# Kernel tuning notes

Measured on AMD Instinct MI355X. Metric: run time of the kernel, lower is better.

Reference implementation:

```python
import jax, jax.numpy as jnp
import numpy as np

B, N, S = 8, 4096, 1024
D1, D2 = 128, 256
IN_C = D1 + D2
MLP = [256, 256]
BN_EPS = 1e-5


def setup_inputs() -> dict:
    key = jax.random.key(0)
    ks = jax.random.split(key, 32)
    inp = {
        'xyz1': jax.random.uniform(ks[0], (B, 3, N), dtype=jnp.float32),
        'xyz2': jax.random.uniform(ks[1], (B, 3, S), dtype=jnp.float32),
        'points1': jax.random.normal(ks[2], (B, D1, N), dtype=jnp.float32),
        'points2': jax.random.normal(ks[3], (B, D2, S), dtype=jnp.float32),
        'colors1': jax.random.normal(ks[4], (B, D1, N), dtype=jnp.float32),
        'colors2': jax.random.normal(ks[5], (B, D2, S), dtype=jnp.float32),
    }
    # conv1x1 + BN params for the two MLP stacks (points / colors)
    k = 6
    last = IN_C
    for li, out_c in enumerate(MLP, start=1):
        for tag in ('p', 'c'):
            scale = 1.0 / np.sqrt(last)
            inp[f'W{tag}{li}'] = jax.random.uniform(ks[k], (out_c, last), jnp.float32, -scale, scale); k += 1
            inp[f'b{tag}{li}'] = jax.random.uniform(ks[k], (out_c,), jnp.float32, -scale, scale); k += 1
            inp[f'g{tag}{li}'] = jnp.ones((out_c,), jnp.float32)
            inp[f'be{tag}{li}'] = jnp.zeros((out_c,), jnp.float32)
        last = out_c
    return inp


def _square_distance(src, dst):
    # src [B,N,3], dst [B,S,3] -> [B,N,S]
    d = -2.0 * jnp.einsum('bnc,bsc->bns', src, dst)
    d = d + jnp.sum(src * src, -1)[:, :, None]
    d = d + jnp.sum(dst * dst, -1)[:, None, :]
    return d


def _three_interp(xyz1, xyz2, feat2):
    # xyz1 [B,N,3], xyz2 [B,S,3], feat2 [B,S,D] -> [B,N,D]
    dists = _square_distance(xyz1, xyz2)              # [B,N,S]
    neg_d3, idx = jax.lax.top_k(-dists, 3)            # smallest 3 distances
    d3 = -neg_d3                                      # [B,N,3] ascending
    recip = 1.0 / (d3 + 1e-8)
    weight = recip / jnp.sum(recip, axis=2, keepdims=True)
    gathered = jax.vmap(lambda f, i: f[i])(feat2, idx)  # [B,N,3,D]
    return jnp.sum(gathered * weight[..., None], axis=2)


def _conv_bn_relu(x, W, b, g, be):
    # x [B,N,Cin]; conv1x1 == per-point linear; BN in training mode (batch stats)
    y = jnp.einsum('bnc,oc->bno', x, W) + b
    m = jnp.mean(y, axis=(0, 1))
    v = jnp.var(y, axis=(0, 1))
    yn = (y - m) * jax.lax.rsqrt(v + BN_EPS)
    return jax.nn.relu(yn * g + be)


def reference(xyz1, xyz2, points1, points2, colors1, colors2,
              Wp1, bp1, gp1, bep1, Wc1, bc1, gc1, bec1,
              Wp2, bp2, gp2, bep2, Wc2, bc2, gc2, bec2):
    x1 = jnp.transpose(xyz1, (0, 2, 1))   # [B,N,3]
    x2 = jnp.transpose(xyz2, (0, 2, 1))   # [B,S,3]
    p2 = jnp.transpose(points2, (0, 2, 1))  # [B,S,D2]
    c2 = jnp.transpose(colors2, (0, 2, 1))

    interp_p = _three_interp(x1, x2, p2)  # [B,N,D2]
    interp_c = _three_interp(x1, x2, c2)

    p1 = jnp.transpose(points1, (0, 2, 1))  # [B,N,D1]
    c1 = jnp.transpose(colors1, (0, 2, 1))
    new_p = jnp.concatenate([p1, interp_p], axis=-1)  # [B,N,IN_C]
    new_c = jnp.concatenate([c1, interp_c], axis=-1)

    new_p = _conv_bn_relu(new_p, Wp1, bp1, gp1, bep1)
    new_p = _conv_bn_relu(new_p, Wp2, bp2, gp2, bep2)
    new_c = _conv_bn_relu(new_c, Wc1, bc1, gc1, bec1)
    new_c = _conv_bn_relu(new_c, Wc2, bc2, gc2, bec2)

    return (jnp.transpose(new_p, (0, 2, 1)), jnp.transpose(new_c, (0, 2, 1)))
```

## Files before the change

### kernel.cpp

```cpp
#include <hip/hip_runtime.h>
#include <cstdint>
#include <cstddef>


#define B_   8
#define N_   4096
#define S_   1024
#define D1_  128
#define D2_  256
#define INC_ 384
#define OC_  256
#define M_   (B_ * N_)

typedef __attribute__((ext_vector_type(8))) short sh8;
typedef __attribute__((ext_vector_type(4))) float f32x4;
typedef __attribute__((ext_vector_type(4))) unsigned short ush4;
typedef __attribute__((ext_vector_type(8))) unsigned short ush8;

__device__ __forceinline__ unsigned short bf16rne(float f) {
    union { float f; unsigned u; } v; v.f = f;
    return (unsigned short)((v.u + 0x7FFFu + ((v.u >> 16) & 1u)) >> 16);
}
__device__ __forceinline__ float bf2f(unsigned short h) {
    union { unsigned u; float f; } v; v.u = ((unsigned)h) << 16;
    return v.f;
}
__device__ __forceinline__ void gload16(const void* gsrc, void* lds) {
    __builtin_amdgcn_global_load_lds(
        (const __attribute__((address_space(1))) void*)gsrc,
        (__attribute__((address_space(3))) void*)lds, 16, 0, 0);
}

#define INS(pd, pi) { \
    bool l0 = (pd < d0) || (pd == d0 && pi < i0); \
    bool l1 = (pd < d1) || (pd == d1 && pi < i1); \
    bool l2 = (pd < d2) || (pd == d2 && pi < i2); \
    d2 = l1 ? d1 : (l2 ? pd : d2);  i2 = l1 ? i1 : (l2 ? pi : i2); \
    d1 = l0 ? d0 : (l1 ? pd : d1);  i1 = l0 ? i0 : (l1 ? pi : i1); \
    d0 = l0 ? pd : d0;              i0 = l0 ? pi : i0; \
}

__global__ __launch_bounds__(256) void front_kernel(
    const float* __restrict__ xyz1, const float* __restrict__ xyz2,
    const float* __restrict__ points1, const float* __restrict__ colors1,
    const float* __restrict__ points2, const float* __restrict__ colors2,
    const float* __restrict__ Wp1, const float* __restrict__ Wc1,
    const float* __restrict__ Wp2, const float* __restrict__ Wc2,
    int* __restrict__ idxo, float* __restrict__ wo,
    unsigned short* __restrict__ p2b, unsigned short* __restrict__ c2b,
    unsigned short* __restrict__ Wb1, unsigned short* __restrict__ Wb2,
    unsigned short* __restrict__ Xp)
{
    __shared__ __align__(16) char fsm[17664];
    const int bid = blockIdx.x;
    const int tid = threadIdx.x;

    if (bid < 1024) {
        float4* sc = (float4*)fsm;
        const int b = bid >> 7, qb = bid & 127;
        const float* x2 = xyz2 + (size_t)b * 3 * S_;
        for (int s = tid; s < S_; s += 256) {
            float xs = x2[s], ys = x2[S_ + s], zs = x2[2 * S_ + s];
            sc[s] = make_float4(xs, ys, zs, xs * xs + ys * ys + zs * zs);
        }
        __syncthreads();
        const int q = qb * 32 + (tid >> 3);
        const int sub = tid & 7;
        const float* x1 = xyz1 + (size_t)b * 3 * N_;
        const float xq = x1[q], yq = x1[N_ + q], zq = x1[2 * N_ + q];
        const float n1 = xq * xq + yq * yq + zq * zq;
        float d0 = 3.4e38f, d1 = 3.4e38f, d2 = 3.4e38f;
        int i0 = 0, i1 = 0, i2 = 0;
#pragma unroll 4
        for (int j = 0; j < 128; ++j) {
            int s = j * 8 + sub;
            float4 v = sc[s];
            float dot = xq * v.x + yq * v.y + zq * v.z;
            float d = (n1 - 2.0f * dot) + v.w;
            bool c0 = d < d0, c1 = d < d1, c2 = d < d2;
            d2 = c1 ? d1 : (c2 ? d : d2); i2 = c1 ? i1 : (c2 ? s : i2);
            d1 = c0 ? d0 : (c1 ? d : d1); i1 = c0 ? i0 : (c1 ? s : i1);
            d0 = c0 ? d : d0;             i0 = c0 ? s : i0;
        }
#pragma unroll
        for (int off = 1; off < 8; off <<= 1) {
            float pd0 = __shfl_xor(d0, off), pd1 = __shfl_xor(d1, off), pd2 = __shfl_xor(d2, off);
            int   pi0 = __shfl_xor(i0, off), pi1 = __shfl_xor(i1, off), pi2 = __shfl_xor(i2, off);
            INS(pd0, pi0) INS(pd1, pi1) INS(pd2, pi2)
        }
        if (sub == 0) {
            float r0 = 1.f / (d0 + 1e-8f);
            float r1 = 1.f / (d1 + 1e-8f);
            float r2 = 1.f / (d2 + 1e-8f);
            float rs = r0 + r1 + r2;
            int base = (b * N_ + q) * 3;
            idxo[base] = i0; idxo[base + 1] = i1; idxo[base + 2] = i2;
            wo[base] = r0 / rs; wo[base + 1] = r1 / rs; wo[base + 2] = r2 / rs;
        }
    } else if (bid < 5120) {
        float (*tile)[33] = (float(*)[33])fsm;
        const int u = bid - 1024;
        const int which = u >> 11;
        const int v = u & 2047;
        const int z = v >> 8, rem = v & 255;
        const int cx = rem & 31, ry = rem >> 5;
        const int tx = tid & 31, ty = tid >> 5;
        const float* s = (which ? colors2 : points2) + (size_t)z * D2_ * S_;
        unsigned short* d = (which ? c2b : p2b) + (size_t)z * S_ * D2_;
#pragma unroll
        for (int i = 0; i < 4; ++i)
            tile[ty + i * 8][tx] = s[(size_t)(ry * 32 + ty + i * 8) * S_ + cx * 32 + tx];
        __syncthreads();
#pragma unroll
        for (int i = 0; i < 4; ++i)
            d[(size_t)(cx * 32 + ty + i * 8) * D2_ + ry * 32 + tx] =
                bf16rne(tile[tx][ty + i * 8]);
    } else if (bid < 5440) {
        int e = ((bid - 5120) * 256 + tid) * 4;
        const float* src; unsigned short* dst; int off;
        if (e < 98304)       { src = Wp1; dst = Wb1;          off = e; }
        else if (e < 196608) { src = Wc1; dst = Wb1 + 98304;  off = e - 98304; }
        else if (e < 262144) { src = Wp2; dst = Wb2;          off = e - 196608; }
        else                 { src = Wc2; dst = Wb2 + 65536;  off = e - 262144; }
        float4 v = *(const float4*)(src + off);
        ush4 o; o[0] = bf16rne(v.x); o[1] = bf16rne(v.y); o[2] = bf16rne(v.z); o[3] = bf16rne(v.w);
        *(ush4*)(dst + off) = o;
    } else {
        float (*tileA)[69] = (float(*)[69])fsm;
        const int u = bid - 5440;
        const int t = u >> 9, rem = u & 511;
        const int b = rem >> 6, n0 = (rem & 63) * 64;
        const float* x1 = t ? colors1 : points1;
        size_t mbase = (size_t)t * M_ + (size_t)b * N_ + n0;
#pragma unroll
        for (int ph = 0; ph < 2; ++ph) {
            if (ph) __syncthreads();
#pragma unroll
            for (int it = 0; it < 4; ++it) {
                int fl4 = it * 256 + tid;
                int dl = fl4 >> 4, nl = (fl4 & 15) * 4;
                float4 v = *(const float4*)(x1 + ((size_t)b * D1_ + ph * 64 + dl) * N_ + n0 + nl);
                tileA[nl][dl] = v.x; tileA[nl + 1][dl] = v.y;
                tileA[nl + 2][dl] = v.z; tileA[nl + 3][dl] = v.w;
            }
            __syncthreads();
#pragma unroll
            for (int it = 0; it < 2; ++it) {
                int e8 = it * 256 + tid;
                int r = e8 >> 3, dc = (e8 & 7) * 8;
                ush8 o;
#pragma unroll
                for (int j = 0; j < 8; ++j) o[j] = bf16rne(tileA[r][dc + j]);
                *(ush8*)(Xp + (mbase + r) * D1_ + ph * 64 + dc) = o;
            }
        }
    }
}

__global__ __launch_bounds__(512, 1) void gemm1f_kernel(
    const unsigned short* __restrict__ Xp,
    const unsigned short* __restrict__ p2b,
    const unsigned short* __restrict__ c2b,
    const int* __restrict__ idxw, const float* __restrict__ wgtw,
    const unsigned short* __restrict__ Wb1,
    unsigned short* __restrict__ Y1,
    float* __restrict__ psum, float* __restrict__ psq)
{
    const int wg  = blockIdx.x;
    const int xcd = wg & 7;
    const int t   = xcd & 1;
    const int mt  = (xcd >> 1) * 32 + (wg >> 3);
    const int m0  = mt * 256;
    const int bb  = m0 >> 12;
    const unsigned short* Aw  = Wb1 + (size_t)t * (OC_ * INC_);
    const unsigned short* Xb  = Xp + (size_t)t * M_ * D1_;
    const unsigned short* f2b = t ? c2b : p2b;

    __shared__ __align__(16) char smem[131072];

    const int tid  = threadIdx.x;
    const int lane = tid & 63;
    const int wid  = tid >> 6;
    const int wc   = wid & 3;
    const int wm   = wid >> 2;
    const int srow = tid >> 3;
    const int k8   = (tid & 7) * 8;
    const int sk   = ((tid & 7) ^ (srow & 7)) * 8;
    const int kgrp = (lane >> 4) * 16;

    int gi[4][3]; float gw[4][3];
#pragma unroll
    for (int p = 0; p < 4; ++p) {
        int base = (m0 + p * 64 + srow) * 3;
#pragma unroll
        for (int j = 0; j < 3; ++j) { gi[p][j] = idxw[base + j]; gw[p][j] = wgtw[base + j]; }
    }

    f32x4 acc[4][8];
#pragma unroll
    for (int i = 0; i < 4; ++i)
#pragma unroll
        for (int j = 0; j < 8; ++j) acc[i][j] = f32x4{0.f, 0.f, 0.f, 0.f};

    auto stageA = [&](int buf, int kc) {
#pragma unroll
        for (int p = 0; p < 4; ++p)
            gload16(Aw + (size_t)(p * 64 + srow) * INC_ + kc + sk,
                    smem + buf * 32768 + p * 8192 + wid * 1024);
    };
    auto stageBX = [&](int buf, int kc) {
#pragma unroll
        for (int p = 0; p < 4; ++p)
            gload16(Xb + (size_t)(m0 + p * 64 + srow) * D1_ + kc + sk,
                    smem + 65536 + buf * 32768 + p * 8192 + wid * 1024);
    };
    auto stageBG = [&](int buf, int kc) {
        const int d0k = kc - D1_ + k8;
#pragma unroll
        for (int p = 0; p < 4; ++p) {
            int row = p * 64 + srow;
            ush8 a0 = *(const ush8*)(f2b + ((size_t)bb * S_ + gi[p][0]) * D2_ + d0k);
            ush8 a1 = *(const ush8*)(f2b + ((size_t)bb * S_ + gi[p][1]) * D2_ + d0k);
            ush8 a2 = *(const ush8*)(f2b + ((size_t)bb * S_ + gi[p][2]) * D2_ + d0k);
            ush8 ov;
#pragma unroll
            for (int j = 0; j < 8; ++j)
                ov[j] = bf16rne(gw[p][0] * bf2f(a0[j]) + gw[p][1] * bf2f(a1[j])
                              + gw[p][2] * bf2f(a2[j]));
            *(ush8*)(smem + 65536 + buf * 32768 + row * 128
                     + ((k8 * 2) ^ ((row & 7) << 4))) = ov;
        }
    };
    auto compute = [&](int buf) {
#pragma unroll
        for (int kk = 0; kk < 2; ++kk) {
            sh8 a[4], b[8];
#pragma unroll
            for (int f = 0; f < 4; ++f) {
                int ra = wc * 64 + (lane & 15) + f * 16;
                a[f] = *(const sh8*)(smem + buf * 32768 + ra * 128
                        + ((kk * 64 + kgrp) ^ ((ra & 7) << 4)));
            }
#pragma unroll
            for (int f = 0; f < 8; ++f) {
                int rb = wm * 128 + (lane & 15) + f * 16;
                b[f] = *(const sh8*)(smem + 65536 + buf * 32768 + rb * 128
                        + ((kk * 64 + kgrp) ^ ((rb & 7) << 4)));
            }
#pragma unroll
            for (int fc = 0; fc < 4; ++fc)
#pragma unroll
                for (int fm = 0; fm < 8; ++fm)
                    acc[fc][fm] = __builtin_amdgcn_mfma_f32_16x16x32_bf16(
                        a[fc], b[fm], acc[fc][fm], 0, 0, 0);
        }
    };

    stageA(0, 0); stageBX(0, 0);
    __syncthreads();
    int cur = 0;
    for (int step = 0; step < 6; ++step) {
        int kcn = (step + 1) * 64;
        if (step < 5) {
            stageA(cur ^ 1, kcn);
            if (kcn < D1_) stageBX(cur ^ 1, kcn);
            else           stageBG(cur ^ 1, kcn);
        }
        compute(cur);
        __syncthreads();
        cur ^= 1;
    }

    const int mrow = m0 + wm * 128 + (lane & 15);
    const int chq  = (lane >> 4) * 4;
#pragma unroll
    for (int fm = 0; fm < 8; ++fm)
#pragma unroll
        for (int fc = 0; fc < 4; ++fc) {
            ush4 v;
#pragma unroll
            for (int r = 0; r < 4; ++r) v[r] = bf16rne(acc[fc][fm][r]);
            *(ush4*)(Y1 + ((size_t)t * M_ + mrow + fm * 16) * OC_
                      + wc * 64 + fc * 16 + chq) = v;
        }

    float* sArr = (float*)smem;
    const int contrib = wm * 16 + (lane & 15);
#pragma unroll
    for (int ph = 0; ph < 2; ++ph) {
#pragma unroll
        for (int fc = 0; fc < 4; ++fc) {
            f32x4 s4;
#pragma unroll
            for (int r = 0; r < 4; ++r) {
                float s = 0.f;
#pragma unroll
                for (int fm = 0; fm < 8; ++fm) { float v = acc[fc][fm][r]; s += ph ? v * v : v; }
                s4[r] = s;
            }
            *(f32x4*)&sArr[contrib * 264 + wc * 64 + fc * 16 + chq] = s4;
        }
        __syncthreads();
        if (tid < 256) {
            float s = 0.f;
#pragma unroll
            for (int k = 0; k < 32; ++k) s += sArr[((k + tid) & 31) * 264 + tid];
            (ph ? psq : psum)[((size_t)t * 128 + mt) * 256 + tid] = s;
        }
        __syncthreads();
    }
}

__global__ __launch_bounds__(256) void reduce_kernel(
    const float* __restrict__ psum, const float* __restrict__ psq,
    const float* __restrict__ gp, const float* __restrict__ bep,
    const float* __restrict__ gc, const float* __restrict__ bec,
    float* __restrict__ ss, int layerOff)
{
    const int t = blockIdx.x, cs = blockIdx.y;
    const int tid = threadIdx.x;
    const int cl = tid & 63, grp = tid >> 6;
    const int c = cs * 64 + cl;
    float s = 0.f, q = 0.f;
    for (int k = grp; k < 128; k += 4) {
        s += psum[((size_t)t * 128 + k) * 256 + c];
        q += psq [((size_t)t * 128 + k) * 256 + c];
    }
    __shared__ float ls[4][64], lq[4][64];
    ls[grp][cl] = s; lq[grp][cl] = q;
    __syncthreads();
    if (tid < 64) {
        s = ls[0][cl] + ls[1][cl] + ls[2][cl] + ls[3][cl];
        q = lq[0][cl] + lq[1][cl] + lq[2][cl] + lq[3][cl];
        float mean = s * (1.f / (float)M_);
        float var  = q * (1.f / (float)M_) - mean * mean;
        float inv  = rsqrtf(var + 1e-5f);
        float g = (t ? gc : gp)[c], be = (t ? bec : bep)[c];
        float sc = g * inv;
        ss[layerOff + t * 256 + c]       = sc;
        ss[layerOff + 512 + t * 256 + c] = be - mean * sc;
    }
}

__global__ __launch_bounds__(512, 1) void gemm2f_kernel(
    const unsigned short* __restrict__ Y1,
    const unsigned short* __restrict__ Wb2,
    const float* __restrict__ ss,
    unsigned short* __restrict__ y2b,
    float* __restrict__ psum, float* __restrict__ psq)
{
    const int t  = blockIdx.y;
    const int m0 = blockIdx.x * 256;
    const unsigned short* Aw = Wb2 + (size_t)t * (OC_ * OC_);
    const unsigned short* By = Y1 + (size_t)t * M_ * OC_;

    __shared__ __align__(16) char smem[131072];
    __shared__ float Slds[256], Hlds[256];

    const int tid  = threadIdx.x;
    const int lane = tid & 63;
    const int wid  = tid >> 6;
    const int wc   = wid & 3;
    const int wm   = wid >> 2;
    const int srow = tid >> 3;
    const int k8   = (tid & 7) * 8;
    const int sk   = ((tid & 7) ^ (srow & 7)) * 8;
    const int kgrp = (lane >> 4) * 16;

    if (tid < 256) { Slds[tid] = ss[t * 256 + tid]; Hlds[tid] = ss[512 + t * 256 + tid]; }
    __syncthreads();

    f32x4 acc[4][8];
#pragma unroll
    for (int i = 0; i < 4; ++i)
#pragma unroll
        for (int j = 0; j < 8; ++j) acc[i][j] = f32x4{0.f, 0.f, 0.f, 0.f};

    auto stageA = [&](int buf, int kc) {
#pragma unroll
        for (int p = 0; p < 4; ++p)
            gload16(Aw + (size_t)(p * 64 + srow) * OC_ + kc + sk,
                    smem + buf * 32768 + p * 8192 + wid * 1024);
    };
    auto stageBY = [&](int buf, int kc) {
#pragma unroll
        for (int p = 0; p < 4; ++p) {
            int row = p * 64 + srow;
            ush8 yv = *(const ush8*)(By + (size_t)(m0 + row) * OC_ + kc + k8);
            ush8 ov;
#pragma unroll
            for (int j = 0; j < 8; ++j) {
                float y = bf2f(yv[j]);
                ov[j] = bf16rne(fmaxf(0.f, fmaf(y, Slds[kc + k8 + j], Hlds[kc + k8 + j])));
            }
            *(ush8*)(smem + 65536 + buf * 32768 + row * 128
                     + ((k8 * 2) ^ ((row & 7) << 4))) = ov;
        }
    };
    auto compute = [&](int buf) {
#pragma unroll
        for (int kk = 0; kk < 2; ++kk) {
            sh8 a[4], b[8];
#pragma unroll
            for (int f = 0; f < 4; ++f) {
                int ra = wc * 64 + (lane & 15) + f * 16;
                a[f] = *(const sh8*)(smem + buf * 32768 + ra * 128
                        + ((kk * 64 + kgrp) ^ ((ra & 7) << 4)));
            }
#pragma unroll
            for (int f = 0; f < 8; ++f) {
                int rb = wm * 128 + (lane & 15) + f * 16;
                b[f] = *(const sh8*)(smem + 65536 + buf * 32768 + rb * 128
                        + ((kk * 64 + kgrp) ^ ((rb & 7) << 4)));
            }
#pragma unroll
            for (int fc = 0; fc < 4; ++fc)
#pragma unroll
                for (int fm = 0; fm < 8; ++fm)
                    acc[fc][fm] = __builtin_amdgcn_mfma_f32_16x16x32_bf16(
                        a[fc], b[fm], acc[fc][fm], 0, 0, 0);
        }
    };

    stageA(0, 0); stageBY(0, 0);
    __syncthreads();
    int cur = 0;
    for (int step = 0; step < 4; ++step) {
        int kcn = (step + 1) * 64;
        if (step < 3) { stageA(cur ^ 1, kcn); stageBY(cur ^ 1, kcn); }
        compute(cur);
        __syncthreads();
        cur ^= 1;
    }

    const int mrow = m0 + wm * 128 + (lane & 15);
    const int chq  = (lane >> 4) * 4;
#pragma unroll
    for (int fm = 0; fm < 8; ++fm)
#pragma unroll
        for (int fc = 0; fc < 4; ++fc) {
            ush4 v;
#pragma unroll
            for (int r = 0; r < 4; ++r) v[r] = bf16rne(acc[fc][fm][r]);
            *(ush4*)(y2b + ((size_t)t * M_ + mrow + fm * 16) * OC_
                      + wc * 64 + fc * 16 + chq) = v;
        }

    float* sArr = (float*)smem;
    const int contrib = wm * 16 + (lane & 15);
#pragma unroll
    for (int ph = 0; ph < 2; ++ph) {
#pragma unroll
        for (int fc = 0; fc < 4; ++fc) {
            f32x4 s4;
#pragma unroll
            for (int r = 0; r < 4; ++r) {
                float s = 0.f;
#pragma unroll
                for (int fm = 0; fm < 8; ++fm) { float v = acc[fc][fm][r]; s += ph ? v * v : v; }
                s4[r] = s;
            }
            *(f32x4*)&sArr[contrib * 264 + wc * 64 + fc * 16 + chq] = s4;
        }
        __syncthreads();
        if (tid < 256) {
            float s = 0.f;
#pragma unroll
            for (int k = 0; k < 32; ++k) s += sArr[((k + tid) & 31) * 264 + tid];
            (ph ? psq : psum)[((size_t)t * 128 + blockIdx.x) * 256 + tid] = s;
        }
        __syncthreads();
    }
}

__global__ __launch_bounds__(256) void bnT_kernel(
    const unsigned short* __restrict__ y2b, const float* __restrict__ ss,
    float* __restrict__ out)
{
    const int z = blockIdx.z;
    const int t = z >> 3, b = z & 7;
    const int o0 = blockIdx.y * 64;
    const int n0 = blockIdx.x * 64;
    const int tid = threadIdx.x;
    __shared__ unsigned short tile[64][72];

    const unsigned short* src = y2b + ((size_t)t * M_ + (size_t)b * N_ + n0) * OC_ + o0;
#pragma unroll
    for (int it = 0; it < 2; ++it) {
        int u = it * 256 + tid;
        int m_l = u >> 3, o8 = (u & 7) * 8;
        *(ush8*)&tile[m_l][o8] = *(const ush8*)(src + (size_t)m_l * OC_ + o8);
    }
    __syncthreads();
#pragma unroll
    for (int it = 0; it < 4; ++it) {
        int v = it * 256 + tid;
        int o_l = v >> 4, n4 = (v & 15) * 4;
        int o = o0 + o_l;
        float sc = ss[1024 + t * 256 + o];
        float sh = ss[1536 + t * 256 + o];
        float4 w;
        w.x = fmaxf(0.f, fmaf(bf2f(tile[n4][o_l]),     sc, sh));
        w.y = fmaxf(0.f, fmaf(bf2f(tile[n4 + 1][o_l]), sc, sh));
        w.z = fmaxf(0.f, fmaf(bf2f(tile[n4 + 2][o_l]), sc, sh));
        w.w = fmaxf(0.f, fmaf(bf2f(tile[n4 + 3][o_l]), sc, sh));
        *(float4*)(out + (((size_t)t * B_ + b) * OC_ + o) * N_ + n0 + n4) = w;
    }
}

extern "C" void kernel_launch(void* const* d_in, const int* in_sizes, int n_in,
                              void* d_out, int out_size, void* d_ws, size_t ws_size,
                              hipStream_t stream)
{
    const float* xyz1    = (const float*)d_in[0];
    const float* xyz2    = (const float*)d_in[1];
    const float* points1 = (const float*)d_in[2];
    const float* points2 = (const float*)d_in[3];
    const float* colors1 = (const float*)d_in[4];
    const float* colors2 = (const float*)d_in[5];
    const float* Wp1  = (const float*)d_in[6];
    const float* gp1  = (const float*)d_in[8];
    const float* bep1 = (const float*)d_in[9];
    const float* Wc1  = (const float*)d_in[10];
    const float* gc1  = (const float*)d_in[12];
    const float* bec1 = (const float*)d_in[13];
    const float* Wp2  = (const float*)d_in[14];
    const float* gp2  = (const float*)d_in[16];
    const float* bep2 = (const float*)d_in[17];
    const float* Wc2  = (const float*)d_in[18];
    const float* gc2  = (const float*)d_in[20];
    const float* bec2 = (const float*)d_in[21];

    char* ws = (char*)d_ws;
    unsigned short* y2b  = (unsigned short*)(ws + 0);
    unsigned short* Xp   = (unsigned short*)(ws + 0);
    unsigned short* p2b  = (unsigned short*)(ws + 16777216);
    unsigned short* c2b  = (unsigned short*)(ws + 20971520);
    int*   idxw = (int*)  (ws + 25165824);
    float* wgtw = (float*)(ws + 25559040);
    unsigned short* Y1   = (unsigned short*)(ws + 33554432);
    unsigned short* Wb1  = (unsigned short*)(ws + 67108864);
    unsigned short* Wb2  = (unsigned short*)(ws + 67895296);
    float* psum = (float*)(ws + 68419584);
    float* psq  = (float*)(ws + 68681728);
    float* ssb  = (float*)(ws + 68943872);
    float* out  = (float*)d_out;

    front_kernel<<<6464, 256, 0, stream>>>(xyz1, xyz2, points1, colors1,
                                           points2, colors2, Wp1, Wc1, Wp2, Wc2,
                                           idxw, wgtw, p2b, c2b, Wb1, Wb2, Xp);
    gemm1f_kernel<<<256, 512, 0, stream>>>(Xp, p2b, c2b, idxw, wgtw,
                                           Wb1, Y1, psum, psq);
    reduce_kernel<<<dim3(2, 4), 256, 0, stream>>>(psum, psq, gp1, bep1, gc1, bec1, ssb, 0);
    gemm2f_kernel<<<dim3(128, 2), 512, 0, stream>>>(Y1, Wb2, ssb, y2b, psum, psq);
    reduce_kernel<<<dim3(2, 4), 256, 0, stream>>>(psum, psq, gp2, bep2, gc2, bec2, ssb, 1024);
    bnT_kernel<<<dim3(64, 4, 16), 256, 0, stream>>>(y2b, ssb, out);
}
```

Before: 113.9 us.

## Fuse BN reductions, second GEMM and transpose into one cooperative kernel

```diff
diff --git a/kernel.cpp b/kernel.cpp
--- a/kernel.cpp
+++ b/kernel.cpp
@@ -1,6 +1,9 @@
 #include <hip/hip_runtime.h>
+#include <hip/hip_cooperative_groups.h>
 #include <cstdint>
 #include <cstddef>
+
+namespace cg = cooperative_groups;
 
 
 #define B_   8
@@ -311,51 +314,29 @@
     }
 }
 
-__global__ __launch_bounds__(256) void reduce_kernel(
-    const float* __restrict__ psum, const float* __restrict__ psq,
-    const float* __restrict__ gp, const float* __restrict__ bep,
-    const float* __restrict__ gc, const float* __restrict__ bec,
-    float* __restrict__ ss, int layerOff)
-{
-    const int t = blockIdx.x, cs = blockIdx.y;
-    const int tid = threadIdx.x;
-    const int cl = tid & 63, grp = tid >> 6;
-    const int c = cs * 64 + cl;
-    float s = 0.f, q = 0.f;
-    for (int k = grp; k < 128; k += 4) {
-        s += psum[((size_t)t * 128 + k) * 256 + c];
-        q += psq [((size_t)t * 128 + k) * 256 + c];
-    }
-    __shared__ float ls[4][64], lq[4][64];
-    ls[grp][cl] = s; lq[grp][cl] = q;
-    __syncthreads();
-    if (tid < 64) {
-        s = ls[0][cl] + ls[1][cl] + ls[2][cl] + ls[3][cl];
-        q = lq[0][cl] + lq[1][cl] + lq[2][cl] + lq[3][cl];
-        float mean = s * (1.f / (float)M_);
-        float var  = q * (1.f / (float)M_) - mean * mean;
-        float inv  = rsqrtf(var + 1e-5f);
-        float g = (t ? gc : gp)[c], be = (t ? bec : bep)[c];
-        float sc = g * inv;
-        ss[layerOff + t * 256 + c]       = sc;
-        ss[layerOff + 512 + t * 256 + c] = be - mean * sc;
-    }
-}
-
-__global__ __launch_bounds__(512, 1) void gemm2f_kernel(
+__global__ __launch_bounds__(512, 1) void gemm2c_kernel(
     const unsigned short* __restrict__ Y1,
     const unsigned short* __restrict__ Wb2,
-    const float* __restrict__ ss,
-    unsigned short* __restrict__ y2b,
-    float* __restrict__ psum, float* __restrict__ psq)
+    const float* __restrict__ psum1, const float* __restrict__ psq1,
+    float* __restrict__ psum2, float* __restrict__ psq2,
+    const float* __restrict__ gp1, const float* __restrict__ bep1,
+    const float* __restrict__ gc1, const float* __restrict__ bec1,
+    const float* __restrict__ gp2, const float* __restrict__ bep2,
+    const float* __restrict__ gc2, const float* __restrict__ bec2,
+    float* __restrict__ out)
 {
-    const int t  = blockIdx.y;
-    const int m0 = blockIdx.x * 256;
+    const int wg  = blockIdx.x;
+    const int xcd = wg & 7;
+    const int t   = xcd & 1;
+    const int mt  = (xcd >> 1) * 32 + (wg >> 3);
+    const int m0  = mt * 256;
+    const int bb  = m0 >> 12;
+    const int n0  = m0 & (N_ - 1);
     const unsigned short* Aw = Wb2 + (size_t)t * (OC_ * OC_);
     const unsigned short* By = Y1 + (size_t)t * M_ * OC_;
 
-    __shared__ __align__(16) char smem[131072];
-    __shared__ float Slds[256], Hlds[256];
+    __shared__ __align__(16) char smem[135168];
+    __shared__ float S1[256], H1[256], S2[256], H2[256];
 
     const int tid  = threadIdx.x;
     const int lane = tid & 63;
@@ -367,8 +348,29 @@
     const int sk   = ((tid & 7) ^ (srow & 7)) * 8;
     const int kgrp = (lane >> 4) * 16;
 
-    if (tid < 256) { Slds[tid] = ss[t * 256 + tid]; Hlds[tid] = ss[512 + t * 256 + tid]; }
-    __syncthreads();
+    {
+        const int ch = tid & 255, half = tid >> 8;
+        float s = 0.f, q = 0.f;
+        for (int k = half * 64; k < half * 64 + 64; ++k) {
+            s += psum1[((size_t)t * 128 + k) * 256 + ch];
+            q += psq1 [((size_t)t * 128 + k) * 256 + ch];
+        }
+        float* sL = (float*)smem;
+        float* qL = sL + 512;
+        sL[half * 256 + ch] = s; qL[half * 256 + ch] = q;
+        __syncthreads();
+        if (tid < 256) {
+            s = sL[tid] + sL[256 + tid];
+            q = qL[tid] + qL[256 + tid];
+            float mean = s * (1.f / (float)M_);
+            float var  = q * (1.f / (float)M_) - mean * mean;
+            float inv  = rsqrtf(var + 1e-5f);
+            float g = (t ? gc1 : gp1)[tid], be = (t ? bec1 : bep1)[tid];
+            float sc = g * inv;
+            S1[tid] = sc; H1[tid] = be - mean * sc;
+        }
+        __syncthreads();
+    }
 
     f32x4 acc[4][8];
 #pragma unroll
@@ -391,7 +393,7 @@
 #pragma unroll
             for (int j = 0; j < 8; ++j) {
                 float y = bf2f(yv[j]);
-                ov[j] = bf16rne(fmaxf(0.f, fmaf(y, Slds[kc + k8 + j], Hlds[kc + k8 + j])));
+                ov[j] = bf16rne(fmaxf(0.f, fmaf(y, S1[kc + k8 + j], H1[kc + k8 + j])));
             }
             *(ush8*)(smem + 65536 + buf * 32768 + row * 128
                      + ((k8 * 2) ^ ((row & 7) << 4))) = ov;
@@ -433,21 +435,9 @@
         cur ^= 1;
     }
 
-    const int mrow = m0 + wm * 128 + (lane & 15);
-    const int chq  = (lane >> 4) * 4;
-#pragma unroll
-    for (int fm = 0; fm < 8; ++fm)
-#pragma unroll
-        for (int fc = 0; fc < 4; ++fc) {
-            ush4 v;
-#pragma unroll
-            for (int r = 0; r < 4; ++r) v[r] = bf16rne(acc[fc][fm][r]);
-            *(ush4*)(y2b + ((size_t)t * M_ + mrow + fm * 16) * OC_
-                      + wc * 64 + fc * 16 + chq) = v;
-        }
-
     float* sArr = (float*)smem;
     const int contrib = wm * 16 + (lane & 15);
+    const int chq = (lane >> 4) * 4;
 #pragma unroll
     for (int ph = 0; ph < 2; ++ph) {
 #pragma unroll
@@ -467,44 +457,63 @@
             float s = 0.f;
 #pragma unroll
             for (int k = 0; k < 32; ++k) s += sArr[((k + tid) & 31) * 264 + tid];
-            (ph ? psq : psum)[((size_t)t * 128 + blockIdx.x) * 256 + tid] = s;
-        }
-        __syncthreads();
-    }
-}
-
-__global__ __launch_bounds__(256) void bnT_kernel(
-    const unsigned short* __restrict__ y2b, const float* __restrict__ ss,
-    float* __restrict__ out)
-{
-    const int z = blockIdx.z;
-    const int t = z >> 3, b = z & 7;
-    const int o0 = blockIdx.y * 64;
-    const int n0 = blockIdx.x * 64;
-    const int tid = threadIdx.x;
-    __shared__ unsigned short tile[64][72];
-
-    const unsigned short* src = y2b + ((size_t)t * M_ + (size_t)b * N_ + n0) * OC_ + o0;
-#pragma unroll
-    for (int it = 0; it < 2; ++it) {
-        int u = it * 256 + tid;
-        int m_l = u >> 3, o8 = (u & 7) * 8;
-        *(ush8*)&tile[m_l][o8] = *(const ush8*)(src + (size_t)m_l * OC_ + o8);
-    }
+            (ph ? psq2 : psum2)[((size_t)t * 128 + mt) * 256 + tid] = s;
+        }
+        __syncthreads();
+    }
+
+    __threadfence();
+    cg::this_grid().sync();
+
+    {
+        const int ch = tid & 255, half = tid >> 8;
+        float s = 0.f, q = 0.f;
+        for (int k = half * 64; k < half * 64 + 64; ++k) {
+            s += psum2[((size_t)t * 128 + k) * 256 + ch];
+            q += psq2 [((size_t)t * 128 + k) * 256 + ch];
+        }
+        float* sL = (float*)smem;
+        float* qL = sL + 512;
+        sL[half * 256 + ch] = s; qL[half * 256 + ch] = q;
+        __syncthreads();
+        if (tid < 256) {
+            s = sL[tid] + sL[256 + tid];
+            q = qL[tid] + qL[256 + tid];
+            float mean = s * (1.f / (float)M_);
+            float var  = q * (1.f / (float)M_) - mean * mean;
+            float inv  = rsqrtf(var + 1e-5f);
+            float g = (t ? gc2 : gp2)[tid], be = (t ? bec2 : bep2)[tid];
+            float sc = g * inv;
+            S2[tid] = sc; H2[tid] = be - mean * sc;
+        }
+        __syncthreads();
+    }
+
+    unsigned short (*tile)[264] = (unsigned short(*)[264])smem;
+#pragma unroll
+    for (int fm = 0; fm < 8; ++fm)
+#pragma unroll
+        for (int fc = 0; fc < 4; ++fc)
+#pragma unroll
+            for (int r = 0; r < 4; ++r) {
+                int o_l = wc * 64 + fc * 16 + chq + r;
+                int n_l = wm * 128 + fm * 16 + (lane & 15);
+                tile[o_l][n_l] = bf16rne(acc[fc][fm][r]);
+            }
     __syncthreads();
-#pragma unroll
-    for (int it = 0; it < 4; ++it) {
-        int v = it * 256 + tid;
-        int o_l = v >> 4, n4 = (v & 15) * 4;
-        int o = o0 + o_l;
-        float sc = ss[1024 + t * 256 + o];
-        float sh = ss[1536 + t * 256 + o];
+    float* ob = out + (((size_t)t * B_ + bb) * OC_) * N_ + n0;
+#pragma unroll
+    for (int it = 0; it < 32; ++it) {
+        int u = it * 512 + tid;
+        int o_l = u >> 6, n4 = (u & 63) * 4;
+        ush4 v = *(const ush4*)&tile[o_l][n4];
+        float sc = S2[o_l], sh = H2[o_l];
         float4 w;
-        w.x = fmaxf(0.f, fmaf(bf2f(tile[n4][o_l]),     sc, sh));
-        w.y = fmaxf(0.f, fmaf(bf2f(tile[n4 + 1][o_l]), sc, sh));
-        w.z = fmaxf(0.f, fmaf(bf2f(tile[n4 + 2][o_l]), sc, sh));
-        w.w = fmaxf(0.f, fmaf(bf2f(tile[n4 + 3][o_l]), sc, sh));
-        *(float4*)(out + (((size_t)t * B_ + b) * OC_ + o) * N_ + n0 + n4) = w;
+        w.x = fmaxf(0.f, fmaf(bf2f(v[0]), sc, sh));
+        w.y = fmaxf(0.f, fmaf(bf2f(v[1]), sc, sh));
+        w.z = fmaxf(0.f, fmaf(bf2f(v[2]), sc, sh));
+        w.w = fmaxf(0.f, fmaf(bf2f(v[3]), sc, sh));
+        *(float4*)(ob + (size_t)o_l * N_ + n4) = w;
     }
 }
 
@@ -532,7 +541,6 @@
     const float* bec2 = (const float*)d_in[21];
 
     char* ws = (char*)d_ws;
-    unsigned short* y2b  = (unsigned short*)(ws + 0);
     unsigned short* Xp   = (unsigned short*)(ws + 0);
     unsigned short* p2b  = (unsigned short*)(ws + 16777216);
     unsigned short* c2b  = (unsigned short*)(ws + 20971520);
@@ -541,18 +549,24 @@
     unsigned short* Y1   = (unsigned short*)(ws + 33554432);
     unsigned short* Wb1  = (unsigned short*)(ws + 67108864);
     unsigned short* Wb2  = (unsigned short*)(ws + 67895296);
-    float* psum = (float*)(ws + 68419584);
-    float* psq  = (float*)(ws + 68681728);
-    float* ssb  = (float*)(ws + 68943872);
+    float* psum1 = (float*)(ws + 68419584);
+    float* psq1  = (float*)(ws + 68681728);
+    float* psum2 = (float*)(ws + 68943872);
+    float* psq2  = (float*)(ws + 69206016);
     float* out  = (float*)d_out;
 
     front_kernel<<<6464, 256, 0, stream>>>(xyz1, xyz2, points1, colors1,
                                            points2, colors2, Wp1, Wc1, Wp2, Wc2,
                                            idxw, wgtw, p2b, c2b, Wb1, Wb2, Xp);
     gemm1f_kernel<<<256, 512, 0, stream>>>(Xp, p2b, c2b, idxw, wgtw,
-                                           Wb1, Y1, psum, psq);
-    reduce_kernel<<<dim3(2, 4), 256, 0, stream>>>(psum, psq, gp1, bep1, gc1, bec1, ssb, 0);
-    gemm2f_kernel<<<dim3(128, 2), 512, 0, stream>>>(Y1, Wb2, ssb, y2b, psum, psq);
-    reduce_kernel<<<dim3(2, 4), 256, 0, stream>>>(psum, psq, gp2, bep2, gc2, bec2, ssb, 1024);
-    bnT_kernel<<<dim3(64, 4, 16), 256, 0, stream>>>(y2b, ssb, out);
-}
+                                           Wb1, Y1, psum1, psq1);
+    {
+        void* args[] = { (void*)&Y1, (void*)&Wb2, (void*)&psum1, (void*)&psq1,
+                         (void*)&psum2, (void*)&psq2,
+                         (void*)&gp1, (void*)&bep1, (void*)&gc1, (void*)&bec1,
+                         (void*)&gp2, (void*)&bep2, (void*)&gc2, (void*)&bec2,
+                         (void*)&out };
+        hipLaunchCooperativeKernel((void*)gemm2c_kernel, dim3(256), dim3(512),
+                                   args, 0, stream);
+    }
+}
```

Result: slower. 169.7 us (+48.9%).

## Shrink GEMM tiles to 128 rows and K-step 32 for higher occupancy

Applied to the files above, without the earlier changes.

```diff
diff --git a/kernel.cpp b/kernel.cpp
--- a/kernel.cpp
+++ b/kernel.cpp
@@ -30,6 +30,7 @@
         (const __attribute__((address_space(1))) void*)gsrc,
         (__attribute__((address_space(3))) void*)lds, 16, 0, 0);
 }
+__device__ __forceinline__ int swzm(int r) { return (r + (r >> 2)) & 3; }
 
 #define INS(pd, pi) { \
     bool l0 = (pd < d0) || (pd == d0 && pi < i0); \
@@ -157,7 +158,7 @@
     }
 }
 
-__global__ __launch_bounds__(512, 1) void gemm1f_kernel(
+__global__ __launch_bounds__(512, 4) void gemm1f_kernel(
     const unsigned short* __restrict__ Xp,
     const unsigned short* __restrict__ p2b,
     const unsigned short* __restrict__ c2b,
@@ -169,99 +170,88 @@
     const int wg  = blockIdx.x;
     const int xcd = wg & 7;
     const int t   = xcd & 1;
-    const int mt  = (xcd >> 1) * 32 + (wg >> 3);
-    const int m0  = mt * 256;
+    const int mt  = (xcd >> 1) * 64 + (wg >> 3);
+    const int m0  = mt * 128;
     const int bb  = m0 >> 12;
     const unsigned short* Aw  = Wb1 + (size_t)t * (OC_ * INC_);
     const unsigned short* Xb  = Xp + (size_t)t * M_ * D1_;
     const unsigned short* f2b = t ? c2b : p2b;
 
-    __shared__ __align__(16) char smem[131072];
+    __shared__ __align__(16) char smem[49152];
 
     const int tid  = threadIdx.x;
     const int lane = tid & 63;
     const int wid  = tid >> 6;
     const int wc   = wid & 3;
     const int wm   = wid >> 2;
-    const int srow = tid >> 3;
-    const int k8   = (tid & 7) * 8;
-    const int sk   = ((tid & 7) ^ (srow & 7)) * 8;
-    const int kgrp = (lane >> 4) * 16;
-
-    int gi[4][3]; float gw[4][3];
-#pragma unroll
-    for (int p = 0; p < 4; ++p) {
-        int base = (m0 + p * 64 + srow) * 3;
-#pragma unroll
-        for (int j = 0; j < 3; ++j) { gi[p][j] = idxw[base + j]; gw[p][j] = wgtw[base + j]; }
-    }
-
-    f32x4 acc[4][8];
+    const int srow = tid >> 2;
+    const int sc_  = tid & 3;
+    const int sk   = (sc_ ^ swzm(srow)) * 8;
+    const int g    = lane >> 4;
+
+    int gi[3]; float gw[3];
+    {
+        int base = (m0 + srow) * 3;
+#pragma unroll
+        for (int j = 0; j < 3; ++j) { gi[j] = idxw[base + j]; gw[j] = wgtw[base + j]; }
+    }
+
+    f32x4 acc[4][4];
 #pragma unroll
     for (int i = 0; i < 4; ++i)
 #pragma unroll
-        for (int j = 0; j < 8; ++j) acc[i][j] = f32x4{0.f, 0.f, 0.f, 0.f};
+        for (int j = 0; j < 4; ++j) acc[i][j] = f32x4{0.f, 0.f, 0.f, 0.f};
 
     auto stageA = [&](int buf, int kc) {
 #pragma unroll
-        for (int p = 0; p < 4; ++p)
-            gload16(Aw + (size_t)(p * 64 + srow) * INC_ + kc + sk,
-                    smem + buf * 32768 + p * 8192 + wid * 1024);
+        for (int p = 0; p < 2; ++p)
+            gload16(Aw + (size_t)(p * 128 + srow) * INC_ + kc + sk,
+                    smem + buf * 24576 + p * 8192 + wid * 1024);
     };
     auto stageBX = [&](int buf, int kc) {
-#pragma unroll
-        for (int p = 0; p < 4; ++p)
-            gload16(Xb + (size_t)(m0 + p * 64 + srow) * D1_ + kc + sk,
-                    smem + 65536 + buf * 32768 + p * 8192 + wid * 1024);
+        gload16(Xb + (size_t)(m0 + srow) * D1_ + kc + sk,
+                smem + buf * 24576 + 16384 + wid * 1024);
     };
     auto stageBG = [&](int buf, int kc) {
-        const int d0k = kc - D1_ + k8;
-#pragma unroll
-        for (int p = 0; p < 4; ++p) {
-            int row = p * 64 + srow;
-            ush8 a0 = *(const ush8*)(f2b + ((size_t)bb * S_ + gi[p][0]) * D2_ + d0k);
-            ush8 a1 = *(const ush8*)(f2b + ((size_t)bb * S_ + gi[p][1]) * D2_ + d0k);
-            ush8 a2 = *(const ush8*)(f2b + ((size_t)bb * S_ + gi[p][2]) * D2_ + d0k);
-            ush8 ov;
-#pragma unroll
-            for (int j = 0; j < 8; ++j)
-                ov[j] = bf16rne(gw[p][0] * bf2f(a0[j]) + gw[p][1] * bf2f(a1[j])
-                              + gw[p][2] * bf2f(a2[j]));
-            *(ush8*)(smem + 65536 + buf * 32768 + row * 128
-                     + ((k8 * 2) ^ ((row & 7) << 4))) = ov;
-        }
+        const int d0k = kc - D1_ + sc_ * 8;
+        ush8 a0 = *(const ush8*)(f2b + ((size_t)bb * S_ + gi[0]) * D2_ + d0k);
+        ush8 a1 = *(const ush8*)(f2b + ((size_t)bb * S_ + gi[1]) * D2_ + d0k);
+        ush8 a2 = *(const ush8*)(f2b + ((size_t)bb * S_ + gi[2]) * D2_ + d0k);
+        ush8 ov;
+#pragma unroll
+        for (int j = 0; j < 8; ++j)
+            ov[j] = bf16rne(gw[0] * bf2f(a0[j]) + gw[1] * bf2f(a1[j])
+                          + gw[2] * bf2f(a2[j]));
+        *(ush8*)(smem + buf * 24576 + 16384 + srow * 64
+                 + ((sc_ ^ swzm(srow)) * 16)) = ov;
     };
     auto compute = [&](int buf) {
-#pragma unroll
-        for (int kk = 0; kk < 2; ++kk) {
-            sh8 a[4], b[8];
-#pragma unroll
-            for (int f = 0; f < 4; ++f) {
-                int ra = wc * 64 + (lane & 15) + f * 16;
-                a[f] = *(const sh8*)(smem + buf * 32768 + ra * 128
-                        + ((kk * 64 + kgrp) ^ ((ra & 7) << 4)));
-            }
-#pragma unroll
-            for (int f = 0; f < 8; ++f) {
-                int rb = wm * 128 + (lane & 15) + f * 16;
-                b[f] = *(const sh8*)(smem + 65536 + buf * 32768 + rb * 128
-                        + ((kk * 64 + kgrp) ^ ((rb & 7) << 4)));
-            }
-#pragma unroll
-            for (int fc = 0; fc < 4; ++fc)
-#pragma unroll
-                for (int fm = 0; fm < 8; ++fm)
-                    acc[fc][fm] = __builtin_amdgcn_mfma_f32_16x16x32_bf16(
-                        a[fc], b[fm], acc[fc][fm], 0, 0, 0);
-        }
+        sh8 a[4], b[4];
+#pragma unroll
+        for (int f = 0; f < 4; ++f) {
+            int ra = wc * 64 + (lane & 15) + f * 16;
+            a[f] = *(const sh8*)(smem + buf * 24576 + ra * 64 + ((g ^ swzm(ra)) * 16));
+        }
+#pragma unroll
+        for (int f = 0; f < 4; ++f) {
+            int rb = wm * 64 + (lane & 15) + f * 16;
+            b[f] = *(const sh8*)(smem + buf * 24576 + 16384 + rb * 64
+                                 + ((g ^ swzm(rb)) * 16));
+        }
+#pragma unroll
+        for (int fc = 0; fc < 4; ++fc)
+#pragma unroll
+            for (int fm = 0; fm < 4; ++fm)
+                acc[fc][fm] = __builtin_amdgcn_mfma_f32_16x16x32_bf16(
+                    a[fc], b[fm], acc[fc][fm], 0, 0, 0);
     };
 
     stageA(0, 0); stageBX(0, 0);
     __syncthreads();
     int cur = 0;
-    for (int step = 0; step < 6; ++step) {
-        int kcn = (step + 1) * 64;
-        if (step < 5) {
+    for (int step = 0; step < 12; ++step) {
+        int kcn = (step + 1) * 32;
+        if (step < 11) {
             stageA(cur ^ 1, kcn);
             if (kcn < D1_) stageBX(cur ^ 1, kcn);
             else           stageBG(cur ^ 1, kcn);
@@ -271,10 +261,10 @@
         cur ^= 1;
     }
 
-    const int mrow = m0 + wm * 128 + (lane & 15);
+    const int mrow = m0 + wm * 64 + (lane & 15);
     const int chq  = (lane >> 4) * 4;
 #pragma unroll
-    for (int fm = 0; fm < 8; ++fm)
+    for (int fm = 0; fm < 4; ++fm)
 #pragma unroll
         for (int fc = 0; fc < 4; ++fc) {
             ush4 v;
@@ -288,6 +278,7 @@
     const int contrib = wm * 16 + (lane & 15);
 #pragma unroll
     for (int ph = 0; ph < 2; ++ph) {
+        __syncthreads();
 #pragma unroll
         for (int fc = 0; fc < 4; ++fc) {
             f32x4 s4;
@@ -295,7 +286,7 @@
             for (int r = 0; r < 4; ++r) {
                 float s = 0.f;
 #pragma unroll
-                for (int fm = 0; fm < 8; ++fm) { float v = acc[fc][fm][r]; s += ph ? v * v : v; }
+                for (int fm = 0; fm < 4; ++fm) { float v = acc[fc][fm][r]; s += ph ? v * v : v; }
                 s4[r] = s;
             }
             *(f32x4*)&sArr[contrib * 264 + wc * 64 + fc * 16 + chq] = s4;
@@ -305,9 +296,8 @@
             float s = 0.f;
 #pragma unroll
             for (int k = 0; k < 32; ++k) s += sArr[((k + tid) & 31) * 264 + tid];
-            (ph ? psq : psum)[((size_t)t * 128 + mt) * 256 + tid] = s;
-        }
-        __syncthreads();
+            (ph ? psq : psum)[((size_t)t * 256 + mt) * 256 + tid] = s;
+        }
     }
 }
 
@@ -322,9 +312,9 @@
     const int cl = tid & 63, grp = tid >> 6;
     const int c = cs * 64 + cl;
     float s = 0.f, q = 0.f;
-    for (int k = grp; k < 128; k += 4) {
-        s += psum[((size_t)t * 128 + k) * 256 + c];
-        q += psq [((size_t)t * 128 + k) * 256 + c];
+    for (int k = grp; k < 256; k += 4) {
+        s += psum[((size_t)t * 256 + k) * 256 + c];
+        q += psq [((size_t)t * 256 + k) * 256 + c];
     }
     __shared__ float ls[4][64], lq[4][64];
     ls[grp][cl] = s; lq[grp][cl] = q;
@@ -342,19 +332,22 @@
     }
 }
 
-__global__ __launch_bounds__(512, 1) void gemm2f_kernel(
+__global__ __launch_bounds__(512, 4) void gemm2f_kernel(
     const unsigned short* __restrict__ Y1,
     const unsigned short* __restrict__ Wb2,
     const float* __restrict__ ss,
     unsigned short* __restrict__ y2b,
     float* __restrict__ psum, float* __restrict__ psq)
 {
-    const int t  = blockIdx.y;
-    const int m0 = blockIdx.x * 256;
+    const int wg  = blockIdx.x;
+    const int xcd = wg & 7;
+    const int t   = xcd & 1;
+    const int mt  = (xcd >> 1) * 64 + (wg >> 3);
+    const int m0  = mt * 128;
     const unsigned short* Aw = Wb2 + (size_t)t * (OC_ * OC_);
     const unsigned short* By = Y1 + (size_t)t * M_ * OC_;
 
-    __shared__ __align__(16) char smem[131072];
+    __shared__ __align__(16) char smem[49152];
     __shared__ float Slds[256], Hlds[256];
 
     const int tid  = threadIdx.x;
@@ -362,81 +355,73 @@
     const int wid  = tid >> 6;
     const int wc   = wid & 3;
     const int wm   = wid >> 2;
-    const int srow = tid >> 3;
-    const int k8   = (tid & 7) * 8;
-    const int sk   = ((tid & 7) ^ (srow & 7)) * 8;
-    const int kgrp = (lane >> 4) * 16;
+    const int srow = tid >> 2;
+    const int sc_  = tid & 3;
+    const int sk   = (sc_ ^ swzm(srow)) * 8;
+    const int g    = lane >> 4;
 
     if (tid < 256) { Slds[tid] = ss[t * 256 + tid]; Hlds[tid] = ss[512 + t * 256 + tid]; }
     __syncthreads();
 
-    f32x4 acc[4][8];
+    f32x4 acc[4][4];
 #pragma unroll
     for (int i = 0; i < 4; ++i)
 #pragma unroll
-        for (int j = 0; j < 8; ++j) acc[i][j] = f32x4{0.f, 0.f, 0.f, 0.f};
+        for (int j = 0; j < 4; ++j) acc[i][j] = f32x4{0.f, 0.f, 0.f, 0.f};
 
     auto stageA = [&](int buf, int kc) {
 #pragma unroll
-        for (int p = 0; p < 4; ++p)
-            gload16(Aw + (size_t)(p * 64 + srow) * OC_ + kc + sk,
-                    smem + buf * 32768 + p * 8192 + wid * 1024);
+        for (int p = 0; p < 2; ++p)
+            gload16(Aw + (size_t)(p * 128 + srow) * OC_ + kc + sk,
+                    smem + buf * 24576 + p * 8192 + wid * 1024);
     };
     auto stageBY = [&](int buf, int kc) {
-#pragma unroll
-        for (int p = 0; p < 4; ++p) {
-            int row = p * 64 + srow;
-            ush8 yv = *(const ush8*)(By + (size_t)(m0 + row) * OC_ + kc + k8);
-            ush8 ov;
-#pragma unroll
-            for (int j = 0; j < 8; ++j) {
-                float y = bf2f(yv[j]);
-                ov[j] = bf16rne(fmaxf(0.f, fmaf(y, Slds[kc + k8 + j], Hlds[kc + k8 + j])));
-            }
-            *(ush8*)(smem + 65536 + buf * 32768 + row * 128
-                     + ((k8 * 2) ^ ((row & 7) << 4))) = ov;
-        }
+        ush8 yv = *(const ush8*)(By + (size_t)(m0 + srow) * OC_ + kc + sc_ * 8);
+        ush8 ov;
+#pragma unroll
+        for (int j = 0; j < 8; ++j) {
+            float y = bf2f(yv[j]);
+            ov[j] = bf16rne(fmaxf(0.f, fmaf(y, Slds[kc + sc_ * 8 + j], Hlds[kc + sc_ * 8 + j])));
+        }
+        *(ush8*)(smem + buf * 24576 + 16384 + srow * 64
+                 + ((sc_ ^ swzm(srow)) * 16)) = ov;
     };
     auto compute = [&](int buf) {
-#pragma unroll
-        for (int kk = 0; kk < 2; ++kk) {
-            sh8 a[4], b[8];
-#pragma unroll
-            for (int f = 0; f < 4; ++f) {
-                int ra = wc * 64 + (lane & 15) + f * 16;
-                a[f] = *(const sh8*)(smem + buf * 32768 + ra * 128
-                        + ((kk * 64 + kgrp) ^ ((ra & 7) << 4)));
-            }
-#pragma unroll
-            for (int f = 0; f < 8; ++f) {
-                int rb = wm * 128 + (lane & 15) + f * 16;
-                b[f] = *(const sh8*)(smem + 65536 + buf * 32768 + rb * 128
-                        + ((kk * 64 + kgrp) ^ ((rb & 7) << 4)));
-            }
-#pragma unroll
-            for (int fc = 0; fc < 4; ++fc)
-#pragma unroll
-                for (int fm = 0; fm < 8; ++fm)
-                    acc[fc][fm] = __builtin_amdgcn_mfma_f32_16x16x32_bf16(
-                        a[fc], b[fm], acc[fc][fm], 0, 0, 0);
-        }
+        sh8 a[4], b[4];
+#pragma unroll
+        for (int f = 0; f < 4; ++f) {
+            int ra = wc * 64 + (lane & 15) + f * 16;
+            a[f] = *(const sh8*)(smem + buf * 24576 + ra * 64 + ((g ^ swzm(ra)) * 16));
+        }
+#pragma unroll
+        for (int f = 0; f < 4; ++f) {
+            int rb = wm * 64 + (lane & 15) + f * 16;
+            b[f] = *(const sh8*)(smem + buf * 24576 + 16384 + rb * 64
+                                 + ((g ^ swzm(rb)) * 16));
+        }
+#pragma unroll
+        for (int fc = 0; fc < 4; ++fc)
+#pragma unroll
+            for (int fm = 0; fm < 4; ++fm)
+                acc[fc][fm] = __builtin_amdgcn_mfma_f32_16x16x32_bf16(
+                    a[fc], b[fm], acc[fc][fm], 0, 0, 0);
     };
 
     stageA(0, 0); stageBY(0, 0);
     __syncthreads();
     int cur = 0;
-    for (int step = 0; step < 4; ++step) {
-        int kcn = (step + 1) * 64;
-        if (step < 3) { stageA(cur ^ 1, kcn); stageBY(cur ^ 1, kcn); }
+    for (int step = 0; step < 8; ++step) {
+        int kcn = (step + 1) * 32;
+        if (step < 7) { stageA(cur ^ 1, kcn); stageBY(cur ^ 1, kcn); }
         compute(cur);
         __syncthreads();
         cur ^= 1;
     }
 
-    const int mrow = m0 + wm * 128 + (lane & 15);
+    const int mrow = m0 + wm * 64 + (lane & 15);
     const int chq  = (lane >> 4) * 4;
 #pragma unroll
-    for (int fm = 0; fm < 8; ++fm)
+    for (int fm = 0; fm < 4; ++fm)
 #pragma unroll
         for (int fc = 0; fc < 4; ++fc) {
             ush4 v;
@@ -450,6 +435,7 @@
     const int contrib = wm * 16 + (lane & 15);
 #pragma unroll
     for (int ph = 0; ph < 2; ++ph) {
+        __syncthreads();
 #pragma unroll
         for (int fc = 0; fc < 4; ++fc) {
             f32x4 s4;
@@ -457,7 +443,7 @@
             for (int r = 0; r < 4; ++r) {
                 float s = 0.f;
 #pragma unroll
-                for (int fm = 0; fm < 8; ++fm) { float v = acc[fc][fm][r]; s += ph ? v * v : v; }
+                for (int fm = 0; fm < 4; ++fm) { float v = acc[fc][fm][r]; s += ph ? v * v : v; }
                 s4[r] = s;
             }
             *(f32x4*)&sArr[contrib * 264 + wc * 64 + fc * 16 + chq] = s4;
@@ -467,9 +453,8 @@
             float s = 0.f;
 #pragma unroll
             for (int k = 0; k < 32; ++k) s += sArr[((k + tid) & 31) * 264 + tid];
-            (ph ? psq : psum)[((size_t)t * 128 + blockIdx.x) * 256 + tid] = s;
-        }
-        __syncthreads();
+            (ph ? psq : psum)[((size_t)t * 256 + mt) * 256 + tid] = s;
+        }
     }
 }
 
@@ -542,17 +527,17 @@
     unsigned short* Wb1  = (unsigned short*)(ws + 67108864);
     unsigned short* Wb2  = (unsigned short*)(ws + 67895296);
     float* psum = (float*)(ws + 68419584);
-    float* psq  = (float*)(ws + 68681728);
-    float* ssb  = (float*)(ws + 68943872);
+    float* psq  = (float*)(ws + 68943872);
+    float* ssb  = (float*)(ws + 69468160);
     float* out  = (float*)d_out;
 
     front_kernel<<<6464, 256, 0, stream>>>(xyz1, xyz2, points1, colors1,
                                            points2, colors2, Wp1, Wc1, Wp2, Wc2,
                                            idxw, wgtw, p2b, c2b, Wb1, Wb2, Xp);
-    gemm1f_kernel<<<256, 512, 0, stream>>>(Xp, p2b, c2b, idxw, wgtw,
+    gemm1f_kernel<<<512, 512, 0, stream>>>(Xp, p2b, c2b, idxw, wgtw,
                                            Wb1, Y1, psum, psq);
     reduce_kernel<<<dim3(2, 4), 256, 0, stream>>>(psum, psq, gp1, bep1, gc1, bec1, ssb, 0);
-    gemm2f_kernel<<<dim3(128, 2), 512, 0, stream>>>(Y1, Wb2, ssb, y2b, psum, psq);
+    gemm2f_kernel<<<512, 512, 0, stream>>>(Y1, Wb2, ssb, y2b, psum, psq);
     reduce_kernel<<<dim3(2, 4), 256, 0, stream>>>(psum, psq, gp2, bep2, gc2, bec2, ssb, 1024);
     bnT_kernel<<<dim3(64, 4, 16), 256, 0, stream>>>(y2b, ssb, out);
 }
```

Result: slower. 134.0 us (+17.6%).

## Fuse layer-1 BN stat reduction into gemm2 and widen kNN split

Applied to the files above, without the earlier changes.

```diff
diff --git a/kernel.cpp b/kernel.cpp
--- a/kernel.cpp
+++ b/kernel.cpp
@@ -55,25 +55,25 @@
     const int bid = blockIdx.x;
     const int tid = threadIdx.x;
 
-    if (bid < 1024) {
+    if (bid < 2048) {
         float4* sc = (float4*)fsm;
-        const int b = bid >> 7, qb = bid & 127;
+        const int b = bid >> 8, qb = bid & 255;
         const float* x2 = xyz2 + (size_t)b * 3 * S_;
         for (int s = tid; s < S_; s += 256) {
             float xs = x2[s], ys = x2[S_ + s], zs = x2[2 * S_ + s];
             sc[s] = make_float4(xs, ys, zs, xs * xs + ys * ys + zs * zs);
         }
         __syncthreads();
-        const int q = qb * 32 + (tid >> 3);
-        const int sub = tid & 7;
+        const int q = qb * 16 + (tid >> 4);
+        const int sub = tid & 15;
         const float* x1 = xyz1 + (size_t)b * 3 * N_;
         const float xq = x1[q], yq = x1[N_ + q], zq = x1[2 * N_ + q];
         const float n1 = xq * xq + yq * yq + zq * zq;
         float d0 = 3.4e38f, d1 = 3.4e38f, d2 = 3.4e38f;
         int i0 = 0, i1 = 0, i2 = 0;
 #pragma unroll 4
-        for (int j = 0; j < 128; ++j) {
-            int s = j * 8 + sub;
+        for (int j = 0; j < 64; ++j) {
+            int s = j * 16 + sub;
             float4 v = sc[s];
             float dot = xq * v.x + yq * v.y + zq * v.z;
             float d = (n1 - 2.0f * dot) + v.w;
@@ -83,7 +83,7 @@
             d0 = c0 ? d : d0;             i0 = c0 ? s : i0;
         }
 #pragma unroll
-        for (int off = 1; off < 8; off <<= 1) {
+        for (int off = 1; off < 16; off <<= 1) {
             float pd0 = __shfl_xor(d0, off), pd1 = __shfl_xor(d1, off), pd2 = __shfl_xor(d2, off);
             int   pi0 = __shfl_xor(i0, off), pi1 = __shfl_xor(i1, off), pi2 = __shfl_xor(i2, off);
             INS(pd0, pi0) INS(pd1, pi1) INS(pd2, pi2)
@@ -97,9 +97,9 @@
             idxo[base] = i0; idxo[base + 1] = i1; idxo[base + 2] = i2;
             wo[base] = r0 / rs; wo[base + 1] = r1 / rs; wo[base + 2] = r2 / rs;
         }
-    } else if (bid < 5120) {
+    } else if (bid < 6144) {
         float (*tile)[33] = (float(*)[33])fsm;
-        const int u = bid - 1024;
+        const int u = bid - 2048;
         const int which = u >> 11;
         const int v = u & 2047;
         const int z = v >> 8, rem = v & 255;
@@ -115,8 +115,8 @@
         for (int i = 0; i < 4; ++i)
             d[(size_t)(cx * 32 + ty + i * 8) * D2_ + ry * 32 + tx] =
                 bf16rne(tile[tx][ty + i * 8]);
-    } else if (bid < 5440) {
-        int e = ((bid - 5120) * 256 + tid) * 4;
+    } else if (bid < 6464) {
+        int e = ((bid - 6144) * 256 + tid) * 4;
         const float* src; unsigned short* dst; int off;
         if (e < 98304)       { src = Wp1; dst = Wb1;          off = e; }
         else if (e < 196608) { src = Wc1; dst = Wb1 + 98304;  off = e - 98304; }
@@ -127,7 +127,7 @@
         *(ush4*)(dst + off) = o;
     } else {
         float (*tileA)[69] = (float(*)[69])fsm;
-        const int u = bid - 5440;
+        const int u = bid - 6464;
         const int t = u >> 9, rem = u & 511;
         const int b = rem >> 6, n0 = (rem & 63) * 64;
         const float* x1 = t ? colors1 : points1;
@@ -345,9 +345,11 @@
 __global__ __launch_bounds__(512, 1) void gemm2f_kernel(
     const unsigned short* __restrict__ Y1,
     const unsigned short* __restrict__ Wb2,
-    const float* __restrict__ ss,
+    const float* __restrict__ psum1, const float* __restrict__ psq1,
+    const float* __restrict__ gp1, const float* __restrict__ bep1,
+    const float* __restrict__ gc1, const float* __restrict__ bec1,
     unsigned short* __restrict__ y2b,
-    float* __restrict__ psum, float* __restrict__ psq)
+    float* __restrict__ psum2, float* __restrict__ psq2)
 {
     const int t  = blockIdx.y;
     const int m0 = blockIdx.x * 256;
@@ -367,8 +369,29 @@
     const int sk   = ((tid & 7) ^ (srow & 7)) * 8;
     const int kgrp = (lane >> 4) * 16;
 
-    if (tid < 256) { Slds[tid] = ss[t * 256 + tid]; Hlds[tid] = ss[512 + t * 256 + tid]; }
-    __syncthreads();
+    {
+        const int ch = tid & 255, half = tid >> 8;
+        float s = 0.f, q = 0.f;
+        for (int k = half * 64; k < half * 64 + 64; ++k) {
+            s += psum1[((size_t)t * 128 + k) * 256 + ch];
+            q += psq1 [((size_t)t * 128 + k) * 256 + ch];
+        }
+        float* sL = (float*)smem;
+        float* qL = sL + 512;
+        sL[half * 256 + ch] = s; qL[half * 256 + ch] = q;
+        __syncthreads();
+        if (tid < 256) {
+            s = sL[tid] + sL[256 + tid];
+            q = qL[tid] + qL[256 + tid];
+            float mean = s * (1.f / (float)M_);
+            float var  = q * (1.f / (float)M_) - mean * mean;
+            float inv  = rsqrtf(var + 1e-5f);
+            float g = (t ? gc1 : gp1)[tid], be = (t ? bec1 : bep1)[tid];
+            float sc = g * inv;
+            Slds[tid] = sc; Hlds[tid] = be - mean * sc;
+        }
+        __syncthreads();
+    }
 
     f32x4 acc[4][8];
 #pragma unroll
@@ -467,7 +490,7 @@
             float s = 0.f;
 #pragma unroll
             for (int k = 0; k < 32; ++k) s += sArr[((k + tid) & 31) * 264 + tid];
-            (ph ? psq : psum)[((size_t)t * 128 + blockIdx.x) * 256 + tid] = s;
+            (ph ? psq2 : psum2)[((size_t)t * 128 + blockIdx.x) * 256 + tid] = s;
         }
         __syncthreads();
     }
@@ -541,18 +564,21 @@
     unsigned short* Y1   = (unsigned short*)(ws + 33554432);
     unsigned short* Wb1  = (unsigned short*)(ws + 67108864);
     unsigned short* Wb2  = (unsigned short*)(ws + 67895296);
-    float* psum = (float*)(ws + 68419584);
-    float* psq  = (float*)(ws + 68681728);
-    float* ssb  = (float*)(ws + 68943872);
+    float* psum1 = (float*)(ws + 68419584);
+    float* psq1  = (float*)(ws + 68681728);
+    float* psum2 = (float*)(ws + 68943872);
+    float* psq2  = (float*)(ws + 69206016);
+    float* ssb   = (float*)(ws + 69468160);
     float* out  = (float*)d_out;
 
-    front_kernel<<<6464, 256, 0, stream>>>(xyz1, xyz2, points1, colors1,
+    front_kernel<<<7488, 256, 0, stream>>>(xyz1, xyz2, points1, colors1,
                                            points2, colors2, Wp1, Wc1, Wp2, Wc2,
                                            idxw, wgtw, p2b, c2b, Wb1, Wb2, Xp);
     gemm1f_kernel<<<256, 512, 0, stream>>>(Xp, p2b, c2b, idxw, wgtw,
-                                           Wb1, Y1, psum, psq);
-    reduce_kernel<<<dim3(2, 4), 256, 0, stream>>>(psum, psq, gp1, bep1, gc1, bec1, ssb, 0);
-    gemm2f_kernel<<<dim3(128, 2), 512, 0, stream>>>(Y1, Wb2, ssb, y2b, psum, psq);
-    reduce_kernel<<<dim3(2, 4), 256, 0, stream>>>(psum, psq, gp2, bep2, gc2, bec2, ssb, 1024);
+                                           Wb1, Y1, psum1, psq1);
+    gemm2f_kernel<<<dim3(128, 2), 512, 0, stream>>>(Y1, Wb2, psum1, psq1,
+                                                    gp1, bep1, gc1, bec1,
+                                                    y2b, psum2, psq2);
+    reduce_kernel<<<dim3(2, 4), 256, 0, stream>>>(psum2, psq2, gp2, bep2, gc2, bec2, ssb, 1024);
     bnT_kernel<<<dim3(64, 4, 16), 256, 0, stream>>>(y2b, ssb, out);
 }
```

New measurement: 125.5 us. +10.1%, slower.
